# Kernel optimization log

Measured on AMD Instinct MI355X. Metric: run time of the kernel, lower is better.

## Reference

```python
import jax, jax.numpy as jnp
import numpy as np

DIM = 1024
HID = 2048
OUT = 1024
NE = 8
TOPK = 2

def _xavier(key, shape):
    fan_in, fan_out = shape[-2], shape[-1]
    lim = jnp.sqrt(6.0 / (fan_in + fan_out))
    return jax.random.uniform(key, shape, jnp.float32, -lim, lim)

def setup_inputs() -> dict:
    key = jax.random.key(0)
    ks = jax.random.split(key, 8)
    X = jax.random.normal(ks[0], (4, 1024, DIM), jnp.float32)
    # stacked expert params: [NE, ...]
    W1 = _xavier(ks[1], (NE, DIM, HID))
    W3 = _xavier(ks[2], (NE, DIM, HID))
    W2 = _xavier(ks[3], (NE, HID, OUT))
    b1 = jnp.zeros((NE, HID), jnp.float32)
    b3 = jnp.zeros((NE, HID), jnp.float32)
    b2 = jnp.zeros((NE, OUT), jnp.float32)
    Wg = _xavier(ks[4], (DIM, NE))
    bg = jnp.zeros((NE,), jnp.float32)
    Wf = _xavier(ks[5], (OUT, OUT))
    bf = jnp.zeros((OUT,), jnp.float32)
    return {"X": X, "W1": W1, "b1": b1, "W3": W3, "b3": b3, "W2": W2, "b2": b2,
            "Wg": Wg, "bg": bg, "Wf": Wf, "bf": bf}

def reference(X, W1, b1, W3, b3, W2, b2, Wg, bg, Wf, bf):
    # gating: [B,S,E]
    gating = jax.nn.softmax(X @ Wg + bg, axis=-1)
    # top-k via argsort (matches original: ascending sort, take last k)
    top_k_indices = jnp.argsort(gating, axis=-1)[..., -TOPK:]  # [B,S,K]
    # dense all-expert SwiGLU FFN: [B,S,E,O]
    h1 = jnp.einsum('bsd,edh->bseh', X, W1) + b1  # [B,S,E,H]
    h3 = jnp.einsum('bsd,edh->bseh', X, W3) + b3
    h = jax.nn.silu(h1 * h3)
    expert_outputs = jnp.einsum('bseh,eho->bseo', h, W2) + b2  # [B,S,E,O]
    # gather top-k expert outputs
    topk_out = jnp.take_along_axis(expert_outputs, top_k_indices[..., None], axis=2)  # [B,S,K,O]
    topk_w = jnp.take_along_axis(gating, top_k_indices, axis=-1)  # [B,S,K]
    mixed = jnp.sum(topk_w[..., None] * topk_out, axis=2)  # [B,S,O]
    return mixed @ Wf + bf
```

## Files before the change

### kernel.cpp

```cpp
#include <hip/hip_runtime.h>

#define DIM  1024
#define HID  2048
#define OUTD 1024
#define NE   8
#define NTOK 4096

using bf16x8 = __attribute__((ext_vector_type(8))) short;
using f32x4  = __attribute__((ext_vector_type(4))) float;

__device__ __forceinline__ unsigned short f2bf(float f) {
  unsigned int u = __builtin_bit_cast(unsigned int, f);
  u += 0x7fff + ((u >> 16) & 1);
  return (unsigned short)(u >> 16);
}
__device__ __forceinline__ float b2f(unsigned short u) {
  unsigned int v = (unsigned int)u << 16;
  return __builtin_bit_cast(float, v);
}

__device__ __forceinline__ void gload16(const void* g, void* l) {
  __builtin_amdgcn_global_load_lds(
      (const __attribute__((address_space(1))) void*)g,
      (__attribute__((address_space(3))) void*)l, 16, 0, 0);
}

__device__ __forceinline__ void tc_tile(const float* __restrict__ inp, int C,
                                        unsigned short* __restrict__ op, int R,
                                        int c0, int r0, float (*tile)[33],
                                        int interleave, int s) {
  int tx = threadIdx.x & 31, ty = threadIdx.x >> 5;
#pragma unroll
  for (int j = 0; j < 4; j++)
    tile[ty + j * 8][tx] = inp[(size_t)(r0 + ty + j * 8) * C + c0 + tx];
  __syncthreads();
  int c = threadIdx.x >> 3, q = threadIdx.x & 7;
  int h = c0 + c;
  int orow = interleave ? (32 * (h >> 4) + 16 * s + (h & 15)) : h;
  ushort4 u;
  u.x = f2bf(tile[q * 4 + 0][c]); u.y = f2bf(tile[q * 4 + 1][c]);
  u.z = f2bf(tile[q * 4 + 2][c]); u.w = f2bf(tile[q * 4 + 3][c]);
  *(ushort4*)&op[(size_t)orow * R + r0 + q * 4] = u;
}

__global__ void tcast_all_kernel(const float* __restrict__ W1, const float* __restrict__ W3,
                                 const float* __restrict__ W2, const float* __restrict__ Wf,
                                 unsigned short* __restrict__ W13t,
                                 unsigned short* __restrict__ W2t,
                                 unsigned short* __restrict__ Wft) {
  __shared__ float tile[32][33];
  int b = blockIdx.x;
  if (b < 32768) {
    int z = b >> 11, rem = b & 2047;
    int e = z & 7, s = z >> 3;
    tc_tile((s ? W3 : W1) + (size_t)e * DIM * HID, HID,
            W13t + (size_t)e * 2 * HID * DIM, DIM,
            (rem & 63) * 32, (rem >> 6) * 32, tile, 1, s);
  } else if (b < 49152) {
    int i = b - 32768;
    int z = i >> 11, rem = i & 2047;
    tc_tile(W2 + (size_t)z * HID * OUTD, OUTD, W2t + (size_t)z * OUTD * HID, HID,
            (rem & 31) * 32, (rem >> 5) * 32, tile, 0, 0);
  } else {
    int i = b - 49152;
    tc_tile(Wf, OUTD, Wft, DIM, (i & 31) * 32, (i >> 5) * 32, tile, 0, 0);
  }
}

__global__ __launch_bounds__(256) void gating_kernel(
    const float* __restrict__ X, const float* __restrict__ Wg,
    const float* __restrict__ bg, unsigned short* __restrict__ Xb,
    int* __restrict__ topk_pack, float* __restrict__ topk_w,
    int* __restrict__ blkcnt) {
  __shared__ float wgs[NE][DIM];
  __shared__ int hist[NE];
  const int tid = threadIdx.x;
  for (int d = tid; d < DIM; d += 256) {
#pragma unroll
    for (int e = 0; e < NE; e++) wgs[e][d] = Wg[d * NE + e];
  }
  if (tid < NE) hist[tid] = 0;
  __syncthreads();
  const int wave = tid >> 6, lane = tid & 63;
  for (int tk = wave; tk < 32; tk += 4) {
    const int t = blockIdx.x * 32 + tk;
    const float* xr = X + (size_t)t * DIM;
    {
      const float4* xp = (const float4*)(xr + lane * 16);
      float4 v0 = xp[0], v1 = xp[1], v2 = xp[2], v3 = xp[3];
      uint4 w0, w1;
      w0.x = f2bf(v0.x) | ((unsigned)f2bf(v0.y) << 16);
      w0.y = f2bf(v0.z) | ((unsigned)f2bf(v0.w) << 16);
      w0.z = f2bf(v1.x) | ((unsigned)f2bf(v1.y) << 16);
      w0.w = f2bf(v1.z) | ((unsigned)f2bf(v1.w) << 16);
      w1.x = f2bf(v2.x) | ((unsigned)f2bf(v2.y) << 16);
      w1.y = f2bf(v2.z) | ((unsigned)f2bf(v2.w) << 16);
      w1.z = f2bf(v3.x) | ((unsigned)f2bf(v3.y) << 16);
      w1.w = f2bf(v3.z) | ((unsigned)f2bf(v3.w) << 16);
      uint4* op2 = (uint4*)(Xb + (size_t)t * DIM + lane * 16);
      op2[0] = w0; op2[1] = w1;
    }
    float acc[NE];
#pragma unroll
    for (int e = 0; e < NE; e++) acc[e] = 0.f;
#pragma unroll
    for (int j = 0; j < 16; j++) {
      float xv = xr[lane + j * 64];
#pragma unroll
      for (int e = 0; e < NE; e++) acc[e] += xv * wgs[e][lane + j * 64];
    }
#pragma unroll
    for (int e = 0; e < NE; e++) {
#pragma unroll
      for (int off = 32; off > 0; off >>= 1) acc[e] += __shfl_xor(acc[e], off, 64);
    }
    if (lane == 0) {
      float p[NE];
      float mx = -1e30f;
#pragma unroll
      for (int e = 0; e < NE; e++) { p[e] = acc[e] + bg[e]; mx = fmaxf(mx, p[e]); }
      float sum = 0.f;
#pragma unroll
      for (int e = 0; e < NE; e++) { p[e] = expf(p[e] - mx); sum += p[e]; }
      float inv = 1.f / sum;
#pragma unroll
      for (int e = 0; e < NE; e++) p[e] *= inv;
      int i1 = 0; float v1 = p[0];
#pragma unroll
      for (int e = 1; e < NE; e++) if (p[e] >= v1) { v1 = p[e]; i1 = e; }
      int i2 = (i1 == 0) ? 1 : 0; float v2 = p[i2];
#pragma unroll
      for (int e = 0; e < NE; e++) {
        if (e == i1) continue;
        if (p[e] >= v2 && e != i2) { v2 = p[e]; i2 = e; }
      }
      topk_pack[t] = i1 | (i2 << 4);
      topk_w[t * 2 + 0] = v1; topk_w[t * 2 + 1] = v2;
      atomicAdd(&hist[i1], 1); atomicAdd(&hist[i2], 1);
    }
  }
  __syncthreads();
  if (tid < NE) blkcnt[blockIdx.x * NE + tid] = hist[tid];
}

__global__ void scatter_kernel(const int* __restrict__ blkcnt,
                               const int* __restrict__ topk_pack,
                               int* __restrict__ counts, int* __restrict__ row_start,
                               int* __restrict__ tp, int* __restrict__ list) {
  __shared__ int lofs[NE];
  const int lane = threadIdx.x;
  const int myb = blockIdx.x;
  int s = 0, t = 0;
#pragma unroll
  for (int e = 0; e < NE; e++) {
    int c0 = blkcnt[lane * NE + e], c1 = blkcnt[(lane + 64) * NE + e];
    int tote = c0 + c1;
    int pre = (lane < myb ? c0 : 0) + (lane + 64 < myb ? c1 : 0);
#pragma unroll
    for (int off = 32; off > 0; off >>= 1) {
      tote += __shfl_xor(tote, off, 64);
      pre  += __shfl_xor(pre,  off, 64);
    }
    if (lane == 0) lofs[e] = s + pre;
    if (myb == 0 && lane == 0) { counts[e] = tote; row_start[e] = s; tp[e] = t; }
    s += tote; t += (tote + 127) >> 7;
  }
  if (myb == 0 && lane == 0) tp[NE] = t;
  __syncthreads();
  if (lane < 32) {
    int tok = myb * 32 + lane;
    int pk = topk_pack[tok];
    int e1 = pk & 15, e2 = (pk >> 4) & 15;
    int p1 = atomicAdd(&lofs[e1], 1); list[p1] = tok << 1;
    int p2 = atomicAdd(&lofs[e2], 1); list[p2] = (tok << 1) | 1;
  }
}

__global__ __launch_bounds__(256, 3) void ffn_a_kernel(
    const unsigned short* __restrict__ Xb,
    const unsigned short* __restrict__ W13t,
    const float* __restrict__ b1, const float* __restrict__ b3,
    const int* __restrict__ counts, const int* __restrict__ row_start,
    const int* __restrict__ tp, const int* __restrict__ list,
    unsigned short* __restrict__ h_buf) {
  __shared__ unsigned short As[128 * 64];
  __shared__ unsigned short Bs[128 * 64];
  const int by = blockIdx.y;
  if (by >= tp[NE]) return;
  int e = 0;
#pragma unroll
  for (int k = 1; k < NE; k++) if (by >= tp[k]) e = k;
  const int ne = counts[e], rs = row_start[e];
  const int m0 = (by - tp[e]) * 128;
  const int n0 = blockIdx.x * 128;

  const int tid = threadIdx.x;
  const int wave = tid >> 6, lane = tid & 63;
  const int lr = lane & 15, lk = lane >> 4;
  const int wm = (wave >> 1) * 64, wn = (wave & 1) * 64;

  const int scs = ((lane & 7) ^ (lane >> 3)) * 8;
  const unsigned short* asrc[4];
  const unsigned short* bsrc[4];
#pragma unroll
  for (int i = 0; i < 4; i++) {
    int sr = (wave * 4 + i) * 8 + (lane >> 3);
    int rr = m0 + sr; if (rr >= ne) rr = m0;
    int tok = list[rs + rr] >> 1;
    asrc[i] = Xb + (size_t)tok * DIM + scs;
    bsrc[i] = W13t + ((size_t)e * 2 * HID + n0 + sr) * DIM + scs;
  }

  f32x4 acc[4][4];
  const f32x4 zero = {0.f, 0.f, 0.f, 0.f};
#pragma unroll
  for (int m = 0; m < 4; m++)
#pragma unroll
    for (int n = 0; n < 4; n++) acc[m][n] = zero;

  const int sx = lr & 7;

  for (int k0 = 0; k0 < DIM; k0 += 64) {
#pragma unroll
    for (int i = 0; i < 4; i++) {
      gload16(asrc[i] + k0, &As[(wave * 4 + i) * 512]);
      gload16(bsrc[i] + k0, &Bs[(wave * 4 + i) * 512]);
    }
    __syncthreads();
#pragma unroll
    for (int kk = 0; kk < 2; kk++) {
      const int sl = ((kk * 4 + lk) ^ sx) * 8;
      bf16x8 a[4], b[4];
#pragma unroll
      for (int m = 0; m < 4; m++)
        a[m] = *(const bf16x8*)&As[(wm + m * 16 + lr) * 64 + sl];
#pragma unroll
      for (int n = 0; n < 4; n++)
        b[n] = *(const bf16x8*)&Bs[(wn + n * 16 + lr) * 64 + sl];
#pragma unroll
      for (int m = 0; m < 4; m++)
#pragma unroll
        for (int n = 0; n < 4; n++)
          acc[m][n] = __builtin_amdgcn_mfma_f32_16x16x32_bf16(a[m], b[n], acc[m][n], 0, 0, 0);
    }
    __syncthreads();
  }

  const int hq = (n0 + wn) >> 5;
#pragma unroll
  for (int g = 0; g < 2; g++) {
    int h = (hq + g) * 16 + lr;
    float b1v = b1[e * HID + h];
    float b3v = b3[e * HID + h];
#pragma unroll
    for (int m = 0; m < 4; m++) {
#pragma unroll
      for (int j = 0; j < 4; j++) {
        int rr = m0 + wm + m * 16 + lk * 4 + j;
        if (rr < ne) {
          float h1 = acc[m][2 * g][j] + b1v;
          float h3 = acc[m][2 * g + 1][j] + b3v;
          float v = h1 * h3;
          h_buf[(size_t)(rs + rr) * HID + h] = f2bf(v / (1.f + expf(-v)));
        }
      }
    }
  }
}

__global__ __launch_bounds__(256, 3) void ffn_b_kernel(
    const unsigned short* __restrict__ h_buf,
    const unsigned short* __restrict__ W2t,
    const float* __restrict__ b2,
    const int* __restrict__ counts, const int* __restrict__ row_start,
    const int* __restrict__ tp, const int* __restrict__ list,
    const float* __restrict__ topk_w, unsigned short* __restrict__ ob) {
  __shared__ unsigned short As[128 * 64];
  __shared__ unsigned short Bs[128 * 64];
  const int by = blockIdx.y;
  if (by >= tp[NE]) return;
  int e = 0;
#pragma unroll
  for (int k = 1; k < NE; k++) if (by >= tp[k]) e = k;
  const int ne = counts[e], rs = row_start[e];
  const int m0 = (by - tp[e]) * 128;
  const int n0 = blockIdx.x * 128;

  const int tid = threadIdx.x;
  const int wave = tid >> 6, lane = tid & 63;
  const int lr = lane & 15, lk = lane >> 4;
  const int wm = (wave >> 1) * 64, wn = (wave & 1) * 64;

  const int scs = ((lane & 7) ^ (lane >> 3)) * 8;
  const unsigned short* asrc[4];
  const unsigned short* bsrc[4];
#pragma unroll
  for (int i = 0; i < 4; i++) {
    int sr = (wave * 4 + i) * 8 + (lane >> 3);
    asrc[i] = h_buf + (size_t)(rs + m0 + sr) * HID + scs;
    bsrc[i] = W2t + ((size_t)e * OUTD + n0 + sr) * HID + scs;
  }

  f32x4 acc[4][4];
  const f32x4 zero = {0.f, 0.f, 0.f, 0.f};
#pragma unroll
  for (int m = 0; m < 4; m++)
#pragma unroll
    for (int n = 0; n < 4; n++) acc[m][n] = zero;

  const int sx = lr & 7;

  for (int k0 = 0; k0 < HID; k0 += 64) {
#pragma unroll
    for (int i = 0; i < 4; i++) {
      gload16(asrc[i] + k0, &As[(wave * 4 + i) * 512]);
      gload16(bsrc[i] + k0, &Bs[(wave * 4 + i) * 512]);
    }
    __syncthreads();
#pragma unroll
    for (int kk = 0; kk < 2; kk++) {
      const int sl = ((kk * 4 + lk) ^ sx) * 8;
      bf16x8 a[4], b[4];
#pragma unroll
      for (int m = 0; m < 4; m++)
        a[m] = *(const bf16x8*)&As[(wm + m * 16 + lr) * 64 + sl];
#pragma unroll
      for (int n = 0; n < 4; n++)
        b[n] = *(const bf16x8*)&Bs[(wn + n * 16 + lr) * 64 + sl];
#pragma unroll
      for (int m = 0; m < 4; m++)
#pragma unroll
        for (int n = 0; n < 4; n++)
          acc[m][n] = __builtin_amdgcn_mfma_f32_16x16x32_bf16(a[m], b[n], acc[m][n], 0, 0, 0);
    }
    __syncthreads();
  }

#pragma unroll
  for (int n = 0; n < 4; n++) {
    int col = n0 + wn + n * 16 + lr;
    float b2v = b2[e * OUTD + col];
#pragma unroll
    for (int m = 0; m < 4; m++) {
#pragma unroll
      for (int j = 0; j < 4; j++) {
        int rr = m0 + wm + m * 16 + lk * 4 + j;
        if (rr < ne) {
          int entry = list[rs + rr];
          float w = topk_w[entry];
          ob[(size_t)entry * OUTD + col] = f2bf(w * (acc[m][n][j] + b2v));
        }
      }
    }
  }
}

__global__ __launch_bounds__(256) void final_kernel(
    const unsigned short* __restrict__ ob, const unsigned short* __restrict__ Wft,
    const float* __restrict__ bfv, float* __restrict__ out) {
  const int bid = blockIdx.x;
  const int n0 = (bid >> 5) * 128;
  const int m0 = ((bid & 7) + 8 * ((bid >> 3) & 3)) * 128;

  __shared__ unsigned short As[128 * 64];
  __shared__ unsigned short Bs[128 * 64];

  const int tid = threadIdx.x;
  const int wave = tid >> 6, lane = tid & 63;
  const int lrow = lane >> 3;
  const int lcol = (lane & 7) * 8;

  const unsigned short* bsrc[4];
#pragma unroll
  for (int i = 0; i < 4; i++) {
    int sr = (wave * 4 + i) * 8 + lrow;
    bsrc[i] = Wft + (size_t)(n0 + sr) * DIM + lcol;
  }

  const int wm = (wave >> 1) * 64, wn = (wave & 1) * 64;
  const int lr = lane & 15, lk = lane >> 4;

  f32x4 acc[4][4];
  const f32x4 zero = {0.f, 0.f, 0.f, 0.f};
#pragma unroll
  for (int m = 0; m < 4; m++)
#pragma unroll
    for (int n = 0; n < 4; n++) acc[m][n] = zero;

  for (int k0 = 0; k0 < DIM; k0 += 64) {
#pragma unroll
    for (int g = 0; g < 8; g++) {
      int idx = g * 256 + tid;
      int r = idx >> 4;
      int c4 = (idx & 15) * 4;
      ushort4 a0 = *(const ushort4*)&ob[((size_t)(m0 + r) * 2) * OUTD + k0 + c4];
      ushort4 a1 = *(const ushort4*)&ob[((size_t)(m0 + r) * 2 + 1) * OUTD + k0 + c4];
      ushort4 u;
      u.x = f2bf(b2f(a0.x) + b2f(a1.x)); u.y = f2bf(b2f(a0.y) + b2f(a1.y));
      u.z = f2bf(b2f(a0.z) + b2f(a1.z)); u.w = f2bf(b2f(a0.w) + b2f(a1.w));
      *(ushort4*)&As[r * 64 + c4] = u;
    }
#pragma unroll
    for (int i = 0; i < 4; i++) gload16(bsrc[i] + k0, &Bs[(wave * 4 + i) * 512]);
    __syncthreads();
#pragma unroll
    for (int kk = 0; kk < 2; kk++) {
      bf16x8 a[4], b[4];
#pragma unroll
      for (int m = 0; m < 4; m++)
        a[m] = *(const bf16x8*)&As[(wm + m * 16 + lr) * 64 + kk * 32 + lk * 8];
#pragma unroll
      for (int n = 0; n < 4; n++)
        b[n] = *(const bf16x8*)&Bs[(wn + n * 16 + lr) * 64 + kk * 32 + lk * 8];
#pragma unroll
      for (int m = 0; m < 4; m++)
#pragma unroll
        for (int n = 0; n < 4; n++)
          acc[m][n] = __builtin_amdgcn_mfma_f32_16x16x32_bf16(a[m], b[n], acc[m][n], 0, 0, 0);
    }
    __syncthreads();
  }

#pragma unroll
  for (int n = 0; n < 4; n++) {
    int col = n0 + wn + n * 16 + lr;
    float bv = bfv[col];
#pragma unroll
    for (int m = 0; m < 4; m++) {
#pragma unroll
      for (int j = 0; j < 4; j++) {
        int r = m0 + wm + m * 16 + lk * 4 + j;
        out[(size_t)r * OUTD + col] = acc[m][n][j] + bv;
      }
    }
  }
}

extern "C" void kernel_launch(void* const* d_in, const int* in_sizes, int n_in,
                              void* d_out, int out_size, void* d_ws, size_t ws_size,
                              hipStream_t stream) {
  const float* X   = (const float*)d_in[0];
  const float* W1  = (const float*)d_in[1];
  const float* b1  = (const float*)d_in[2];
  const float* W3  = (const float*)d_in[3];
  const float* b3  = (const float*)d_in[4];
  const float* W2  = (const float*)d_in[5];
  const float* b2  = (const float*)d_in[6];
  const float* Wg  = (const float*)d_in[7];
  const float* bg  = (const float*)d_in[8];
  const float* Wf  = (const float*)d_in[9];
  const float* bfv = (const float*)d_in[10];
  float* out = (float*)d_out;

  char* p = (char*)d_ws;
  auto alloc = [&](size_t bytes) { char* r = p; p += (bytes + 255) & ~(size_t)255; return r; };
  unsigned short* Xb   = (unsigned short*)alloc((size_t)NTOK * DIM * 2);
  unsigned short* W13t = (unsigned short*)alloc((size_t)NE * 2 * HID * DIM * 2);
  unsigned short* W2t  = (unsigned short*)alloc((size_t)NE * OUTD * HID * 2);
  unsigned short* Wft  = (unsigned short*)alloc((size_t)OUTD * DIM * 2);
  unsigned short* hbuf = (unsigned short*)alloc((size_t)(NTOK * 2 + 256) * HID * 2);
  unsigned short* ob   = (unsigned short*)alloc((size_t)NTOK * 2 * OUTD * 2);
  int* topk_pack       = (int*)alloc(NTOK * 4);
  float* topk_w        = (float*)alloc(NTOK * 2 * 4);
  int* counts          = (int*)alloc(NE * 4);
  int* row_start       = (int*)alloc(NE * 4);
  int* tp              = (int*)alloc((NE + 1) * 4);
  int* blkcnt          = (int*)alloc(128 * NE * 4);
  int* list            = (int*)alloc(NTOK * 2 * 4);

  gating_kernel<<<128, 256, 0, stream>>>(X, Wg, bg, Xb, topk_pack, topk_w, blkcnt);
  tcast_all_kernel<<<50176, 256, 0, stream>>>(W1, W3, W2, Wf, W13t, W2t, Wft);

  scatter_kernel<<<128, 64, 0, stream>>>(blkcnt, topk_pack, counts, row_start, tp, list);

  ffn_a_kernel<<<dim3(2 * HID / 128, 72), 256, 0, stream>>>(
      Xb, W13t, b1, b3, counts, row_start, tp, list, hbuf);
  ffn_b_kernel<<<dim3(OUTD / 128, 72), 256, 0, stream>>>(
      hbuf, W2t, b2, counts, row_start, tp, list, topk_w, ob);
  final_kernel<<<256, 256, 0, stream>>>(ob, Wft, bfv, out);
}
```

Measured before the change: 302.6 us.

## Fold W2/Wf transpose-cast into ffn_a launch and double gating block count

The W2 and Wf transpose-to-bf16 work moves out of the standalone cast kernel and into extra blocks appended to the ffn_a grid, so it can run alongside the gated-expert GEMM instead of before it. The ffn_a grid becomes 1D, and the cast blocks reuse the As shared buffer as their tile. Gating and scatter now handle 16 tokens per block across 256 blocks, giving more parallelism in those small kernels. The risk is that cast blocks compete with GEMM blocks for CUs and bandwidth, and the trailing cast blocks could lengthen the ffn_a tail.

```diff
diff --git a/kernel.cpp b/kernel.cpp
--- a/kernel.cpp
+++ b/kernel.cpp
@@ -43,28 +43,15 @@
   *(ushort4*)&op[(size_t)orow * R + r0 + q * 4] = u;
 }
 
-__global__ void tcast_all_kernel(const float* __restrict__ W1, const float* __restrict__ W3,
-                                 const float* __restrict__ W2, const float* __restrict__ Wf,
-                                 unsigned short* __restrict__ W13t,
-                                 unsigned short* __restrict__ W2t,
-                                 unsigned short* __restrict__ Wft) {
+__global__ void tcast_w13_kernel(const float* __restrict__ W1, const float* __restrict__ W3,
+                                 unsigned short* __restrict__ W13t) {
   __shared__ float tile[32][33];
   int b = blockIdx.x;
-  if (b < 32768) {
-    int z = b >> 11, rem = b & 2047;
-    int e = z & 7, s = z >> 3;
-    tc_tile((s ? W3 : W1) + (size_t)e * DIM * HID, HID,
-            W13t + (size_t)e * 2 * HID * DIM, DIM,
-            (rem & 63) * 32, (rem >> 6) * 32, tile, 1, s);
-  } else if (b < 49152) {
-    int i = b - 32768;
-    int z = i >> 11, rem = i & 2047;
-    tc_tile(W2 + (size_t)z * HID * OUTD, OUTD, W2t + (size_t)z * OUTD * HID, HID,
-            (rem & 31) * 32, (rem >> 5) * 32, tile, 0, 0);
-  } else {
-    int i = b - 49152;
-    tc_tile(Wf, OUTD, Wft, DIM, (i & 31) * 32, (i >> 5) * 32, tile, 0, 0);
-  }
+  int z = b >> 11, rem = b & 2047;
+  int e = z & 7, s = z >> 3;
+  tc_tile((s ? W3 : W1) + (size_t)e * DIM * HID, HID,
+          W13t + (size_t)e * 2 * HID * DIM, DIM,
+          (rem & 63) * 32, (rem >> 6) * 32, tile, 1, s);
 }
 
 __global__ __launch_bounds__(256) void gating_kernel(
@@ -82,8 +69,8 @@
   if (tid < NE) hist[tid] = 0;
   __syncthreads();
   const int wave = tid >> 6, lane = tid & 63;
-  for (int tk = wave; tk < 32; tk += 4) {
-    const int t = blockIdx.x * 32 + tk;
+  for (int tk = wave; tk < 16; tk += 4) {
+    const int t = blockIdx.x * 16 + tk;
     const float* xr = X + (size_t)t * DIM;
     {
       const float4* xp = (const float4*)(xr + lane * 16);
@@ -153,9 +140,14 @@
   int s = 0, t = 0;
 #pragma unroll
   for (int e = 0; e < NE; e++) {
-    int c0 = blkcnt[lane * NE + e], c1 = blkcnt[(lane + 64) * NE + e];
-    int tote = c0 + c1;
-    int pre = (lane < myb ? c0 : 0) + (lane + 64 < myb ? c1 : 0);
+    int tote = 0, pre = 0;
+#pragma unroll
+    for (int j = 0; j < 4; j++) {
+      int b = lane * 4 + j;
+      int c = blkcnt[b * NE + e];
+      tote += c;
+      if (b < myb) pre += c;
+    }
 #pragma unroll
     for (int off = 32; off > 0; off >>= 1) {
       tote += __shfl_xor(tote, off, 64);
@@ -167,8 +159,8 @@
   }
   if (myb == 0 && lane == 0) tp[NE] = t;
   __syncthreads();
-  if (lane < 32) {
-    int tok = myb * 32 + lane;
+  if (lane < 16) {
+    int tok = myb * 16 + lane;
     int pk = topk_pack[tok];
     int e1 = pk & 15, e2 = (pk >> 4) & 15;
     int p1 = atomicAdd(&lofs[e1], 1); list[p1] = tok << 1;
@@ -176,23 +168,41 @@
   }
 }
 
+#define FFNA_BLKS 2304
+#define W2T_BLKS  16384
 __global__ __launch_bounds__(256, 3) void ffn_a_kernel(
     const unsigned short* __restrict__ Xb,
     const unsigned short* __restrict__ W13t,
     const float* __restrict__ b1, const float* __restrict__ b3,
+    const float* __restrict__ W2, const float* __restrict__ Wf,
+    unsigned short* __restrict__ W2t, unsigned short* __restrict__ Wft,
     const int* __restrict__ counts, const int* __restrict__ row_start,
     const int* __restrict__ tp, const int* __restrict__ list,
     unsigned short* __restrict__ h_buf) {
   __shared__ unsigned short As[128 * 64];
   __shared__ unsigned short Bs[128 * 64];
-  const int by = blockIdx.y;
+  const int bid = blockIdx.x;
+  if (bid >= FFNA_BLKS) {
+    int i = bid - FFNA_BLKS;
+    if (i < W2T_BLKS) {
+      int z = i >> 11, rem = i & 2047;
+      tc_tile(W2 + (size_t)z * HID * OUTD, OUTD, W2t + (size_t)z * OUTD * HID, HID,
+              (rem & 31) * 32, (rem >> 5) * 32, (float(*)[33])As, 0, 0);
+    } else {
+      int i2 = i - W2T_BLKS;
+      tc_tile(Wf, OUTD, Wft, DIM, (i2 & 31) * 32, (i2 >> 5) * 32,
+              (float(*)[33])As, 0, 0);
+    }
+    return;
+  }
+  const int by = bid >> 5;
   if (by >= tp[NE]) return;
   int e = 0;
 #pragma unroll
   for (int k = 1; k < NE; k++) if (by >= tp[k]) e = k;
   const int ne = counts[e], rs = row_start[e];
   const int m0 = (by - tp[e]) * 128;
-  const int n0 = blockIdx.x * 128;
+  const int n0 = (bid & 31) * 128;
 
   const int tid = threadIdx.x;
   const int wave = tid >> 6, lane = tid & 63;
@@ -465,16 +475,16 @@
   int* counts          = (int*)alloc(NE * 4);
   int* row_start       = (int*)alloc(NE * 4);
   int* tp              = (int*)alloc((NE + 1) * 4);
-  int* blkcnt          = (int*)alloc(128 * NE * 4);
+  int* blkcnt          = (int*)alloc(256 * NE * 4);
   int* list            = (int*)alloc(NTOK * 2 * 4);
 
-  gating_kernel<<<128, 256, 0, stream>>>(X, Wg, bg, Xb, topk_pack, topk_w, blkcnt);
-  tcast_all_kernel<<<50176, 256, 0, stream>>>(W1, W3, W2, Wf, W13t, W2t, Wft);
-
-  scatter_kernel<<<128, 64, 0, stream>>>(blkcnt, topk_pack, counts, row_start, tp, list);
-
-  ffn_a_kernel<<<dim3(2 * HID / 128, 72), 256, 0, stream>>>(
-      Xb, W13t, b1, b3, counts, row_start, tp, list, hbuf);
+  gating_kernel<<<256, 256, 0, stream>>>(X, Wg, bg, Xb, topk_pack, topk_w, blkcnt);
+  tcast_w13_kernel<<<32768, 256, 0, stream>>>(W1, W3, W13t);
+
+  scatter_kernel<<<256, 64, 0, stream>>>(blkcnt, topk_pack, counts, row_start, tp, list);
+
+  ffn_a_kernel<<<FFNA_BLKS + W2T_BLKS + 1024, 256, 0, stream>>>(
+      Xb, W13t, b1, b3, W2, Wf, W2t, Wft, counts, row_start, tp, list, hbuf);
   ffn_b_kernel<<<dim3(OUTD / 128, 72), 256, 0, stream>>>(
       hbuf, W2t, b2, counts, row_start, tp, list, topk_w, ob);
   final_kernel<<<256, 256, 0, stream>>>(ob, Wft, bfv, out);
```

Result: faster. 281.2 us (-7.1%).
